# Optimization experiments

Measured on AMD Instinct MI355X. Metric: run time of the kernel, lower is better.

Reference implementation:

```python
import jax, jax.numpy as jnp
import numpy as np

B, S, NX, NH = 4, 1024, 1024, 16
HD = NX // NH  # head_features = 64


def setup_inputs() -> dict:
    key = jax.random.key(0)
    k1, k2, k3 = jax.random.split(key, 3)
    x = jax.random.normal(k1, (B, S, NX), dtype=jnp.float32)
    w_attn = 0.02 * jax.random.normal(k2, (NX, 3 * NX), dtype=jnp.float32)
    b_attn = jnp.zeros((3 * NX,), dtype=jnp.float32)
    w_proj = 0.02 * jax.random.normal(k3, (NX, NX), dtype=jnp.float32)
    b_proj = jnp.zeros((NX,), dtype=jnp.float32)
    causal_bias = jnp.tril(jnp.ones((S, S), dtype=jnp.float32))  # tril buffer
    return {"x": x, "w_attn": w_attn, "b_attn": b_attn,
            "w_proj": w_proj, "b_proj": b_proj, "causal_bias": causal_bias}


def reference(x, w_attn, b_attn, w_proj, b_proj, causal_bias):
    # c_attn: fused qkv projection (Conv1D == addmm)
    qkv = x @ w_attn + b_attn                     # [B, S, 3*NX]
    q, k, v = jnp.split(qkv, 3, axis=-1)          # each [B, S, NX]
    # split heads -> [B, H, S, D]
    q = q.reshape(B, S, NH, HD).transpose(0, 2, 1, 3)
    k = k.reshape(B, S, NH, HD).transpose(0, 2, 1, 3)
    v = v.reshape(B, S, NH, HD).transpose(0, 2, 1, 3)
    # present: stack of (key in [B,H,S,D] layout, value)
    present = jnp.stack((k, v))                   # [2, B, H, S, D]
    # scores with scale=True
    w = jnp.einsum('bhqd,bhkd->bhqk', q, k) / jnp.sqrt(jnp.float32(HD))
    b = causal_bias[None, None, :, :]             # [1,1,S,S] (nd==ns==S)
    w = w * b - 1e10 * (1.0 - b)                  # multiplicative mask trick
    p = jax.nn.softmax(w, axis=-1)
    a = jnp.einsum('bhqk,bhkd->bhqd', p, v)       # [B, H, S, D]
    a = a.transpose(0, 2, 1, 3).reshape(B, S, NX)  # merge heads
    out = a @ w_proj + b_proj                     # c_proj
    return out, present
```

## Files before the change

kernel.cpp:

```cpp
#include <hip/hip_runtime.h>
#include <hip/hip_bf16.h>

typedef __attribute__((ext_vector_type(8))) short short8;
typedef __attribute__((ext_vector_type(4))) float floatx4;

constexpr int Bsz = 4, Ssz = 1024, NXc = 1024, NHc = 16, HDc = 64;
constexpr int OUT_ELEMS  = Bsz * Ssz * NXc;
constexpr int HEAD_ELEMS = Bsz * NHc * Ssz * HDc;

union BF8 { __hip_bfloat16 h[8]; uint4 v; short8 s; };

__device__ __forceinline__ uint4 cvt8(const float* __restrict__ p) {
    float4 a = *reinterpret_cast<const float4*>(p);
    float4 b = *reinterpret_cast<const float4*>(p + 4);
    BF8 u;
    u.h[0] = __float2bfloat16(a.x); u.h[1] = __float2bfloat16(a.y);
    u.h[2] = __float2bfloat16(a.z); u.h[3] = __float2bfloat16(a.w);
    u.h[4] = __float2bfloat16(b.x); u.h[5] = __float2bfloat16(b.y);
    u.h[6] = __float2bfloat16(b.z); u.h[7] = __float2bfloat16(b.w);
    return u.v;
}

__device__ __forceinline__ void load_lds_16B(const void* g, void* l) {
    __builtin_amdgcn_global_load_lds(
        (const __attribute__((address_space(1))) unsigned int*)g,
        (__attribute__((address_space(3))) unsigned int*)l, 16, 0, 0);
}


__global__ __launch_bounds__(256) void prep_kernel(
    const float* __restrict__ x, __hip_bfloat16* __restrict__ x_bf,
    const float* __restrict__ w_attn, __hip_bfloat16* __restrict__ wTa,
    const float* __restrict__ w_proj, __hip_bfloat16* __restrict__ wTp)
{
    const int bid = blockIdx.x, tid = threadIdx.x;
    __shared__ float t[64][65];
    if (bid < 2048) {
        const int i = (bid * 256 + tid) * 8;
        *reinterpret_cast<uint4*>(x_bf + i) = cvt8(x + i);
        return;
    }
    const float* in; __hip_bfloat16* outp; int N, bx, by;
    if (bid < 2816) { const int q = bid - 2048; in = w_attn; outp = wTa; N = 3072; bx = q % 48; by = q / 48; }
    else            { const int q = bid - 2816; in = w_proj; outp = wTp; N = 1024; bx = q % 16; by = q / 16; }
    const int k0 = by * 64, n0 = bx * 64;
#pragma unroll
    for (int j = 0; j < 16; ++j) {
        const int idx = tid + j * 256;
        const int row = idx >> 6, col = idx & 63;
        t[row][col] = in[(size_t)(k0 + row) * N + n0 + col];
    }
    __syncthreads();
#pragma unroll
    for (int j = 0; j < 16; ++j) {
        const int idx = tid + j * 256;
        const int orow = idx >> 6, ocol = idx & 63;
        outp[(size_t)(n0 + orow) * 1024 + k0 + ocol] = __float2bfloat16(t[ocol][orow]);
    }
}

template <int EPI>
__global__ __launch_bounds__(256) void gemm128p(
    const __hip_bfloat16* __restrict__ A,
    const __hip_bfloat16* __restrict__ Bt,
    const float* __restrict__ bias,
    float* __restrict__ outf,
    __hip_bfloat16* __restrict__ qws,
    float* __restrict__ present,
    __hip_bfloat16* __restrict__ kws,
    __hip_bfloat16* __restrict__ vtws,
    int M, int N, int K)
{
    __shared__ __align__(16) __hip_bfloat16 As[3][4096];
    __shared__ __align__(16) __hip_bfloat16 Bs[3][4096];

    const int tid  = threadIdx.x;
    const int w    = tid >> 6, lane = tid & 63;
    const int quad = lane >> 4, l16 = lane & 15;
    const int m0 = blockIdx.y * 128, n0 = blockIdx.x * 128;
    const int mb = (w >> 1) * 64, nbw = (w & 1) * 64;

    const int srow = lane >> 2;
    const int sksw = (((lane & 3) ^ ((lane >> 3) & 3))) * 8;

    const int rsw = (l16 >> 1) & 3;

    floatx4 acc[4][4];
#pragma unroll
    for (int i = 0; i < 4; ++i)
#pragma unroll
        for (int j = 0; j < 4; ++j)
#pragma unroll
            for (int r = 0; r < 4; ++r) acc[i][j][r] = 0.f;

    auto stage = [&](int buf, int k0) {
#pragma unroll
        for (int c = 0; c < 2; ++c) {
            const int chunk = w * 2 + c;
            const int row = chunk * 16 + srow;
            load_lds_16B(A + (size_t)(m0 + row) * K + k0 + sksw,
                         &As[buf][chunk * 512]);
            load_lds_16B(Bt + (size_t)(n0 + row) * K + k0 + sksw,
                         &Bs[buf][chunk * 512]);
        }
    };

    stage(0, 0);
    int cb = 0;
    for (int k0 = 0; k0 < K; k0 += 32) {
        if (k0 + 32 < K) {
            const int nb_ = (cb == 2) ? 0 : cb + 1;
            stage(nb_, k0 + 32);
            asm volatile("s_waitcnt vmcnt(4)" ::: "memory");
        } else {
            asm volatile("s_waitcnt vmcnt(0)" ::: "memory");
        }
        __builtin_amdgcn_s_barrier();
        __builtin_amdgcn_sched_barrier(0);

        short8 af[4], bfr[4];
#pragma unroll
        for (int mi = 0; mi < 4; ++mi)
            af[mi] = *reinterpret_cast<const short8*>(
                &As[cb][(mb + mi * 16 + l16) * 32 + ((quad ^ rsw) * 8)]);
#pragma unroll
        for (int ni = 0; ni < 4; ++ni)
            bfr[ni] = *reinterpret_cast<const short8*>(
                &Bs[cb][(nbw + ni * 16 + l16) * 32 + ((quad ^ rsw) * 8)]);
        __builtin_amdgcn_s_setprio(1);
#pragma unroll
        for (int mi = 0; mi < 4; ++mi)
#pragma unroll
            for (int ni = 0; ni < 4; ++ni)
                acc[mi][ni] = __builtin_amdgcn_mfma_f32_16x16x32_bf16(
                    af[mi], bfr[ni], acc[mi][ni], 0, 0, 0);
        __builtin_amdgcn_s_setprio(0);

        cb = (cb == 2) ? 0 : cb + 1;
    }

#pragma unroll
    for (int mi = 0; mi < 4; ++mi) {
#pragma unroll
        for (int ni = 0; ni < 4; ++ni) {
            const int col = n0 + nbw + ni * 16 + l16;
            const float bsv = bias[col];
#pragma unroll
            for (int r = 0; r < 4; ++r) {
                const int row = m0 + mb + mi * 16 + quad * 4 + r;
                const float v = acc[mi][ni][r] + bsv;
                if (EPI == 0) {
                    const int seg = col >> 10;
                    const int c = col & 1023;
                    if (seg == 0) {
                        qws[(size_t)row * 1024 + c] = __float2bfloat16(v);
                    } else {
                        const int bq = row >> 10, s = row & 1023;
                        const int hh = c >> 6, d = c & 63;
                        const size_t idx =
                            ((size_t)((bq * 16 + hh) * 1024 + s)) * 64 + d;
                        const int kt = s >> 6, key = s & 63;
                        const size_t tbase =
                            ((size_t)((bq * 16 + hh) * 16 + kt)) * 4096;
                        if (seg == 1) {
                            present[idx] = v;
                            kws[tbase + key * 64 +
                                ((((d >> 3) ^ (key & 7)) << 3) | (d & 7))] =
                                __float2bfloat16(v);
                        } else {
                            present[HEAD_ELEMS + idx] = v;
                            vtws[tbase + d * 64 +
                                ((((key >> 3) ^ (d & 7)) << 3) | (key & 7))] =
                                __float2bfloat16(v);
                        }
                    }
                } else {
                    outf[(size_t)row * N + col] = v;
                }
            }
        }
    }
}

__global__ __launch_bounds__(256) void attn_v4(
    const __hip_bfloat16* __restrict__ q_ws,
    const __hip_bfloat16* __restrict__ k_ws,
    const __hip_bfloat16* __restrict__ vt_ws,
    __hip_bfloat16* __restrict__ a_ws)
{
    const int bx = blockIdx.x, h = blockIdx.y, b = blockIdx.z;
    const int tid  = threadIdx.x;
    const int wave = tid >> 6, lane = tid & 63;
    const int quad = lane >> 4, l16 = lane & 15;
    const int stripe = wave * 16;

    const int bh = b * 16 + h;
    const __hip_bfloat16* Kbase = k_ws  + (size_t)bh * 65536;
    const __hip_bfloat16* Vbase = vt_ws + (size_t)bh * 65536;

    __shared__ __align__(16) __hip_bfloat16 Ksf[3][4096];
    __shared__ __align__(16) __hip_bfloat16 Vsf[3][4096];
    __shared__ __align__(16) __hip_bfloat16 Ps[64][72];

    constexpr float SCL = 0.18033688011f;

#pragma unroll
    for (int pass = 0; pass < 2; ++pass) {
        const int qt = (pass == 0) ? (8 + bx) : (7 - bx);

        const __hip_bfloat16* Qb =
            q_ws + ((size_t)(b * Ssz + qt * 64 + stripe + l16)) * NXc + h * 64;
        const short8 qf0 = *reinterpret_cast<const short8*>(Qb + quad * 8);
        const short8 qf1 = *reinterpret_cast<const short8*>(Qb + 32 + quad * 8);

        float m_i[4], l_i[4];
#pragma unroll
        for (int r = 0; r < 4; ++r) { m_i[r] = -1e9f; l_i[r] = 0.f; }
        floatx4 oacc[4];
#pragma unroll
        for (int ni = 0; ni < 4; ++ni)
#pragma unroll
            for (int r = 0; r < 4; ++r) oacc[ni][r] = 0.f;

#pragma unroll
        for (int c2 = 0; c2 < 2; ++c2) {
            const int c = wave + c2 * 4;
            load_lds_16B(Kbase + c * 512 + (lane << 3), &Ksf[0][c * 512]);
            load_lds_16B(Vbase + c * 512 + (lane << 3), &Vsf[0][c * 512]);
        }

        int cw = 0;
        for (int kt = 0; kt <= qt; ++kt) {
            if (kt < qt) {
                const int nb_ = (cw == 2) ? 0 : cw + 1;
                const __hip_bfloat16* Kt = Kbase + (size_t)(kt + 1) * 4096;
                const __hip_bfloat16* Vt = Vbase + (size_t)(kt + 1) * 4096;
#pragma unroll
                for (int c2 = 0; c2 < 2; ++c2) {
                    const int c = wave + c2 * 4;
                    load_lds_16B(Kt + c * 512 + (lane << 3), &Ksf[nb_][c * 512]);
                    load_lds_16B(Vt + c * 512 + (lane << 3), &Vsf[nb_][c * 512]);
                }
                asm volatile("s_waitcnt vmcnt(4)" ::: "memory");
            } else {
                asm volatile("s_waitcnt vmcnt(0)" ::: "memory");
            }
            __builtin_amdgcn_s_barrier();
            __builtin_amdgcn_sched_barrier(0);

            floatx4 sacc[4];
#pragma unroll
            for (int ni = 0; ni < 4; ++ni)
#pragma unroll
                for (int r = 0; r < 4; ++r) sacc[ni][r] = 0.f;
            __builtin_amdgcn_s_setprio(1);
#pragma unroll
            for (int ni = 0; ni < 4; ++ni) {
                const int key = ni * 16 + l16;
                const int sw = key & 7;
                const short8 kf0 = *reinterpret_cast<const short8*>(
                    &Ksf[cw][key * 64 + ((quad ^ sw) << 3)]);
                const short8 kf1 = *reinterpret_cast<const short8*>(
                    &Ksf[cw][key * 64 + (((4 + quad) ^ sw) << 3)]);
                sacc[ni] = __builtin_amdgcn_mfma_f32_16x16x32_bf16(
                    qf0, kf0, sacc[ni], 0, 0, 0);
                sacc[ni] = __builtin_amdgcn_mfma_f32_16x16x32_bf16(
                    qf1, kf1, sacc[ni], 0, 0, 0);
            }
            __builtin_amdgcn_s_setprio(0);

            const bool diag = (kt == qt);
            float alpha_[4];
#pragma unroll
            for (int r = 0; r < 4; ++r) {
                const int lrow = stripe + quad * 4 + r;
                float sv[4];
                float mx = -1e30f;
#pragma unroll
                for (int ni = 0; ni < 4; ++ni) {
                    float v = sacc[ni][r] * SCL;
                    if (diag && (ni * 16 + l16) > lrow) v = -1e9f;
                    sv[ni] = v;
                    mx = fmaxf(mx, v);
                }
                mx = fmaxf(mx, __shfl_xor(mx, 1));
                mx = fmaxf(mx, __shfl_xor(mx, 2));
                mx = fmaxf(mx, __shfl_xor(mx, 4));
                mx = fmaxf(mx, __shfl_xor(mx, 8));
                const float mnew = fmaxf(m_i[r], mx);
                const float al = exp2f(m_i[r] - mnew);
                m_i[r] = mnew;
                float s = 0.f;
#pragma unroll
                for (int nn = 0; nn < 4; ++nn) {
                    const int ni = (nn + quad) & 3;
                    const float p = exp2f(sv[ni] - mnew);
                    s += p;
                    Ps[lrow][ni * 16 + l16] = __float2bfloat16(p);
                }
                s += __shfl_xor(s, 1);
                s += __shfl_xor(s, 2);
                s += __shfl_xor(s, 4);
                s += __shfl_xor(s, 8);
                l_i[r] = l_i[r] * al + s;
                alpha_[r] = al;
            }

#pragma unroll
            for (int ni = 0; ni < 4; ++ni)
#pragma unroll
                for (int r = 0; r < 4; ++r) oacc[ni][r] *= alpha_[r];

            __builtin_amdgcn_s_setprio(1);
#pragma unroll
            for (int kk = 0; kk < 64; kk += 32) {
                const short8 pf = *reinterpret_cast<const short8*>(
                    &Ps[stripe + l16][kk + quad * 8]);
#pragma unroll
                for (int ni = 0; ni < 4; ++ni) {
                    const int d = ni * 16 + l16;
                    const int chunk = (kk >> 3) + quad;
                    const short8 vf = *reinterpret_cast<const short8*>(
                        &Vsf[cw][d * 64 + ((chunk ^ (d & 7)) << 3)]);
                    oacc[ni] = __builtin_amdgcn_mfma_f32_16x16x32_bf16(
                        pf, vf, oacc[ni], 0, 0, 0);
                }
            }
            __builtin_amdgcn_s_setprio(0);

            cw = (cw == 2) ? 0 : cw + 1;
        }

        __builtin_amdgcn_s_barrier();

#pragma unroll
        for (int ni = 0; ni < 4; ++ni) {
#pragma unroll
            for (int r = 0; r < 4; ++r) {
                const int row = qt * 64 + stripe + quad * 4 + r;
                const int col = h * 64 + ni * 16 + l16;
                const float inv = 1.0f / fmaxf(l_i[r], 1e-20f);
                a_ws[((size_t)(b * Ssz + row)) * NXc + col] =
                    __float2bfloat16(oacc[ni][r] * inv);
            }
        }
    }
}

template <int EPI>
__global__ __launch_bounds__(256) void gemm64(
    const void* __restrict__ Av, const float* __restrict__ Bw,
    const float* __restrict__ bias, float* __restrict__ out0,
    float* __restrict__ present, int M, int N, int K)
{
    __shared__ __align__(16) __hip_bfloat16 As[64][40];
    __shared__ __align__(16) __hip_bfloat16 Bs[64][40];
    const int tid = threadIdx.x;
    const int wave = tid >> 6, lane = tid & 63;
    const int quad = lane >> 4, l16 = lane & 15;
    const int m0 = blockIdx.y * 64, n0 = blockIdx.x * 64;
    const int mb = (wave >> 1) * 32, nb = (wave & 1) * 32;
    const int arow = tid >> 2, aseg = tid & 3;
    const int brow = tid >> 3, bseg = tid & 7;
    floatx4 acc[2][2];
#pragma unroll
    for (int i = 0; i < 2; ++i)
#pragma unroll
        for (int j = 0; j < 2; ++j)
#pragma unroll
            for (int r = 0; r < 4; ++r) acc[i][j][r] = 0.f;
    for (int k0 = 0; k0 < K; k0 += 32) {
        if (EPI == 0) {
            const float* A = (const float*)Av;
            *reinterpret_cast<uint4*>(&As[arow][aseg * 8]) =
                cvt8(A + (size_t)(m0 + arow) * K + k0 + aseg * 8);
        } else {
            const __hip_bfloat16* A = (const __hip_bfloat16*)Av;
            *reinterpret_cast<uint4*>(&As[arow][aseg * 8]) =
                *reinterpret_cast<const uint4*>(
                    A + (size_t)(m0 + arow) * K + k0 + aseg * 8);
        }
        const float* bp = Bw + (size_t)(k0 + brow) * N + n0 + bseg * 8;
        float4 b0 = *reinterpret_cast<const float4*>(bp);
        float4 b1 = *reinterpret_cast<const float4*>(bp + 4);
        Bs[bseg * 8 + 0][brow] = __float2bfloat16(b0.x);
        Bs[bseg * 8 + 1][brow] = __float2bfloat16(b0.y);
        Bs[bseg * 8 + 2][brow] = __float2bfloat16(b0.z);
        Bs[bseg * 8 + 3][brow] = __float2bfloat16(b0.w);
        Bs[bseg * 8 + 4][brow] = __float2bfloat16(b1.x);
        Bs[bseg * 8 + 5][brow] = __float2bfloat16(b1.y);
        Bs[bseg * 8 + 6][brow] = __float2bfloat16(b1.z);
        Bs[bseg * 8 + 7][brow] = __float2bfloat16(b1.w);
        __syncthreads();
        short8 af[2], bf[2];
#pragma unroll
        for (int mm = 0; mm < 2; ++mm)
            af[mm] = *reinterpret_cast<const short8*>(&As[mb + mm * 16 + l16][quad * 8]);
#pragma unroll
        for (int nn = 0; nn < 2; ++nn)
            bf[nn] = *reinterpret_cast<const short8*>(&Bs[nb + nn * 16 + l16][quad * 8]);
#pragma unroll
        for (int mm = 0; mm < 2; ++mm)
#pragma unroll
            for (int nn = 0; nn < 2; ++nn)
                acc[mm][nn] = __builtin_amdgcn_mfma_f32_16x16x32_bf16(
                    af[mm], bf[nn], acc[mm][nn], 0, 0, 0);
        __syncthreads();
    }
#pragma unroll
    for (int mm = 0; mm < 2; ++mm)
#pragma unroll
        for (int nn = 0; nn < 2; ++nn) {
            const int col = n0 + nb + nn * 16 + l16;
            const float bsv = bias[col];
#pragma unroll
            for (int r = 0; r < 4; ++r) {
                const int row = m0 + mb + mm * 16 + quad * 4 + r;
                const float v = acc[mm][nn][r] + bsv;
                if (EPI == 0) {
                    const int seg = col >> 10;
                    const int c = col & 1023;
                    if (seg == 0) out0[(size_t)row * 1024 + c] = v;
                    else {
                        const int b = row >> 10, s = row & 1023;
                        const int h = c >> 6, d = c & 63;
                        const size_t idx = ((size_t)((b * 16 + h) * 1024 + s)) * 64 + d;
                        if (seg == 1) present[idx] = v;
                        else          present[HEAD_ELEMS + idx] = v;
                    }
                } else out0[(size_t)row * N + col] = v;
            }
        }
}

__global__ __launch_bounds__(256) void attn64(
    const float* __restrict__ qbuf, const float* __restrict__ present,
    __hip_bfloat16* __restrict__ a_ws)
{
    const int qt = blockIdx.x, h = blockIdx.y, b = blockIdx.z;
    const int tid = threadIdx.x;
    const int wave = tid >> 6, lane = tid & 63;
    const int quad = lane >> 4, l16 = lane & 15;
    const int mb = (wave >> 1) * 32, nb = (wave & 1) * 32;
    const size_t headoff = ((size_t)(b * 16 + h)) * Ssz * HDc;
    const float* Qb = qbuf + ((size_t)(b * Ssz + qt * 64)) * NXc + h * 64;
    const float* Kp = present + headoff;
    const float* Vp = present + HEAD_ELEMS + headoff;
    __shared__ __align__(16) __hip_bfloat16 Qs[64][72];
    __shared__ __align__(16) __hip_bfloat16 Ks[64][72];
    __shared__ __align__(16) __hip_bfloat16 Vts[64][72];
    __shared__ __align__(16) __hip_bfloat16 Ps[64][72];
    __shared__ float Sc[64][65];
    __shared__ float mrow[64], lrow[64], arw[64];
#pragma unroll
    for (int it = 0; it < 2; ++it) {
        const int c = tid + it * 256;
        const int row = c >> 3, seg = c & 7;
        *reinterpret_cast<uint4*>(&Qs[row][seg * 8]) =
            cvt8(Qb + (size_t)row * NXc + seg * 8);
    }
    if (tid < 64) { mrow[tid] = -1e9f; lrow[tid] = 0.f; }
    floatx4 oacc[2][2];
#pragma unroll
    for (int i = 0; i < 2; ++i)
#pragma unroll
        for (int j = 0; j < 2; ++j)
#pragma unroll
            for (int r = 0; r < 4; ++r) oacc[i][j][r] = 0.f;
    __syncthreads();
    for (int kt = 0; kt <= qt; ++kt) {
#pragma unroll
        for (int it = 0; it < 2; ++it) {
            const int c = tid + it * 256;
            const int row = c >> 3, seg = c & 7;
            *reinterpret_cast<uint4*>(&Ks[row][seg * 8]) =
                cvt8(Kp + (size_t)(kt * 64 + row) * 64 + seg * 8);
            const float* vp = Vp + (size_t)(kt * 64 + row) * 64 + seg * 8;
            float4 v0 = *reinterpret_cast<const float4*>(vp);
            float4 v1 = *reinterpret_cast<const float4*>(vp + 4);
            Vts[seg * 8 + 0][row] = __float2bfloat16(v0.x);
            Vts[seg * 8 + 1][row] = __float2bfloat16(v0.y);
            Vts[seg * 8 + 2][row] = __float2bfloat16(v0.z);
            Vts[seg * 8 + 3][row] = __float2bfloat16(v0.w);
            Vts[seg * 8 + 4][row] = __float2bfloat16(v1.x);
            Vts[seg * 8 + 5][row] = __float2bfloat16(v1.y);
            Vts[seg * 8 + 6][row] = __float2bfloat16(v1.z);
            Vts[seg * 8 + 7][row] = __float2bfloat16(v1.w);
        }
        __syncthreads();
        floatx4 sacc[2][2];
#pragma unroll
        for (int i = 0; i < 2; ++i)
#pragma unroll
            for (int j = 0; j < 2; ++j)
#pragma unroll
                for (int r = 0; r < 4; ++r) sacc[i][j][r] = 0.f;
#pragma unroll
        for (int kd = 0; kd < 64; kd += 32) {
            short8 af[2], bf[2];
#pragma unroll
            for (int mm = 0; mm < 2; ++mm)
                af[mm] = *reinterpret_cast<const short8*>(&Qs[mb + mm * 16 + l16][kd + quad * 8]);
#pragma unroll
            for (int nn = 0; nn < 2; ++nn)
                bf[nn] = *reinterpret_cast<const short8*>(&Ks[nb + nn * 16 + l16][kd + quad * 8]);
#pragma unroll
            for (int mm = 0; mm < 2; ++mm)
#pragma unroll
                for (int nn = 0; nn < 2; ++nn)
                    sacc[mm][nn] = __builtin_amdgcn_mfma_f32_16x16x32_bf16(
                        af[mm], bf[nn], sacc[mm][nn], 0, 0, 0);
        }
        const bool diag = (kt == qt);
#pragma unroll
        for (int mm = 0; mm < 2; ++mm)
#pragma unroll
            for (int nn = 0; nn < 2; ++nn)
#pragma unroll
                for (int r = 0; r < 4; ++r) {
                    const int row = mb + mm * 16 + quad * 4 + r;
                    const int col = nb + nn * 16 + l16;
                    float v = fminf(fmaxf(sacc[mm][nn][r] * 0.125f, -1e8f), 1e8f);
                    if (diag && col > row) v = -1e9f;
                    Sc[row][col] = v;
                }
        __syncthreads();
        if (tid < 64) {
            const int r = tid;
            const float mo = mrow[r];
            float mx = mo;
            for (int c = 0; c < 64; ++c) mx = fmaxf(mx, Sc[r][c]);
            const float al = (mo <= -5e8f) ? 0.f : __expf(mo - mx);
            float sum = 0.f;
            for (int c = 0; c < 64; ++c) {
                const float sv = Sc[r][c];
                const float p = (sv <= -5e8f) ? 0.f : __expf(sv - mx);
                sum += p;
                Ps[r][c] = __float2bfloat16(p);
            }
            mrow[r] = mx;
            lrow[r] = lrow[r] * al + sum;
            arw[r]  = al;
        }
        __syncthreads();
#pragma unroll
        for (int mm = 0; mm < 2; ++mm) {
            const int rbase = mb + mm * 16 + quad * 4;
#pragma unroll
            for (int r = 0; r < 4; ++r) {
                const float al = arw[rbase + r];
                oacc[mm][0][r] *= al;
                oacc[mm][1][r] *= al;
            }
        }
#pragma unroll
        for (int kk = 0; kk < 64; kk += 32) {
            short8 pf[2], vf[2];
#pragma unroll
            for (int mm = 0; mm < 2; ++mm)
                pf[mm] = *reinterpret_cast<const short8*>(&Ps[mb + mm * 16 + l16][kk + quad * 8]);
#pragma unroll
            for (int nn = 0; nn < 2; ++nn)
                vf[nn] = *reinterpret_cast<const short8*>(&Vts[nb + nn * 16 + l16][kk + quad * 8]);
#pragma unroll
            for (int mm = 0; mm < 2; ++mm)
#pragma unroll
                for (int nn = 0; nn < 2; ++nn)
                    oacc[mm][nn] = __builtin_amdgcn_mfma_f32_16x16x32_bf16(
                        pf[mm], vf[nn], oacc[mm][nn], 0, 0, 0);
        }
        __syncthreads();
    }
#pragma unroll
    for (int mm = 0; mm < 2; ++mm)
#pragma unroll
        for (int nn = 0; nn < 2; ++nn)
#pragma unroll
            for (int r = 0; r < 4; ++r) {
                const int row = mb + mm * 16 + quad * 4 + r;
                const int col = nb + nn * 16 + l16;
                const float inv = 1.0f / fmaxf(lrow[row], 1e-20f);
                a_ws[((size_t)(b * Ssz + qt * 64 + row)) * NXc + h * 64 + col] =
                    __float2bfloat16(oacc[mm][nn][r] * inv);
            }
}

extern "C" void kernel_launch(void* const* d_in, const int* in_sizes, int n_in,
                              void* d_out, int out_size, void* d_ws, size_t ws_size,
                              hipStream_t stream) {
    const float* x      = (const float*)d_in[0];
    const float* w_attn = (const float*)d_in[1];
    const float* b_attn = (const float*)d_in[2];
    const float* w_proj = (const float*)d_in[3];
    const float* b_proj = (const float*)d_in[4];

    float* out     = (float*)d_out;
    float* present = out + OUT_ELEMS;

    const size_t NEED = 32u * 1024u * 1024u;
    if (ws_size >= NEED) {
        __hip_bfloat16* reg1 = (__hip_bfloat16*)d_ws;
        __hip_bfloat16* reg2 = reg1 + 4194304;
        __hip_bfloat16* reg3 = reg2 + 4194304;
        __hip_bfloat16* wTa  = reg3 + 4194304;
        __hip_bfloat16* wTp  = wTa + 3145728;
        __hip_bfloat16* kws  = (__hip_bfloat16*)out;
        __hip_bfloat16* vtws = kws + 4194304;

        prep_kernel<<<3072, 256, 0, stream>>>(x, reg1, w_attn, wTa, w_proj, wTp);

        gemm128p<0><<<dim3(24, 32), 256, 0, stream>>>(
            reg1, wTa, b_attn, nullptr, reg2, present, kws, vtws,
            4096, 3072, 1024);

        attn_v4<<<dim3(8, 16, 4), 256, 0, stream>>>(reg2, kws, vtws, reg2);

        gemm128p<1><<<dim3(8, 32), 256, 0, stream>>>(
            reg2, wTp, b_proj, out, nullptr, nullptr, nullptr, nullptr,
            4096, 1024, 1024);
    } else {
        __hip_bfloat16* a_ws = (__hip_bfloat16*)d_ws;
        hipMemsetAsync(d_ws, 0, (size_t)OUT_ELEMS * sizeof(__hip_bfloat16), stream);
        gemm64<0><<<dim3(48, 64), 256, 0, stream>>>(x, w_attn, b_attn, out, present,
                                                    4096, 3072, 1024);
        attn64<<<dim3(16, 16, 4), 256, 0, stream>>>(out, present, a_ws);
        gemm64<1><<<dim3(16, 64), 256, 0, stream>>>(a_ws, w_proj, b_proj, out, nullptr,
                                                    4096, 1024, 1024);
    }
}
```

Before: 199.9 us.

## Swizzle GEMM/attention block order and split attention into one q-tile per block

The GEMMs now launch a 1D grid and remap block IDs with an XCD-aware swizzle (wg&7 striding), so neighbouring tiles share an XCD and its L2. The attention kernel drops the two-pass paired q-tile scheme. It launches one block per (b,h,q-tile), heaviest tiles first, with the same XCD swizzle, and cuts the LDS ring from three buffers to two with a full vmcnt(0) wait each iteration. This buys finer-grained load balancing and lower LDS use, which may allow more resident blocks. The cost is less overlap of the K/V prefetch with compute.

After: 213.7 us. 1.07x slower.

```diff
diff --git a/kernel.cpp b/kernel.cpp
--- a/kernel.cpp
+++ b/kernel.cpp
@@ -74,15 +74,20 @@
     __shared__ __align__(16) __hip_bfloat16 As[3][4096];
     __shared__ __align__(16) __hip_bfloat16 Bs[3][4096];
 
+    const int nbx = N >> 7;
+    const int nwg = (M >> 7) * nbx;
+    const int wg  = blockIdx.x;
+    const int swz = (wg & 7) * (nwg >> 3) + (wg >> 3);
+    const int by  = swz / nbx, bx = swz % nbx;
+
     const int tid  = threadIdx.x;
     const int w    = tid >> 6, lane = tid & 63;
     const int quad = lane >> 4, l16 = lane & 15;
-    const int m0 = blockIdx.y * 128, n0 = blockIdx.x * 128;
+    const int m0 = by * 128, n0 = bx * 128;
     const int mb = (w >> 1) * 64, nbw = (w & 1) * 64;
 
     const int srow = lane >> 2;
     const int sksw = (((lane & 3) ^ ((lane >> 3) & 3))) * 8;
-
     const int rsw = (l16 >> 1) & 3;
 
     floatx4 acc[4][4];
@@ -182,167 +187,163 @@
     }
 }
 
-__global__ __launch_bounds__(256) void attn_v4(
+__global__ __launch_bounds__(256) void attn_v5(
     const __hip_bfloat16* __restrict__ q_ws,
     const __hip_bfloat16* __restrict__ k_ws,
     const __hip_bfloat16* __restrict__ vt_ws,
     __hip_bfloat16* __restrict__ a_ws)
 {
-    const int bx = blockIdx.x, h = blockIdx.y, b = blockIdx.z;
+    const int wg  = blockIdx.x;
+    const int swz = (wg & 7) * 128 + (wg >> 3);
+    const int qt  = 15 - (swz & 15);
+    const int bh  = swz >> 4;
+    const int b = bh >> 4, h = bh & 15;
+
     const int tid  = threadIdx.x;
     const int wave = tid >> 6, lane = tid & 63;
     const int quad = lane >> 4, l16 = lane & 15;
     const int stripe = wave * 16;
 
-    const int bh = b * 16 + h;
     const __hip_bfloat16* Kbase = k_ws  + (size_t)bh * 65536;
     const __hip_bfloat16* Vbase = vt_ws + (size_t)bh * 65536;
 
-    __shared__ __align__(16) __hip_bfloat16 Ksf[3][4096];
-    __shared__ __align__(16) __hip_bfloat16 Vsf[3][4096];
+    __shared__ __align__(16) __hip_bfloat16 Ksf[2][4096];
+    __shared__ __align__(16) __hip_bfloat16 Vsf[2][4096];
     __shared__ __align__(16) __hip_bfloat16 Ps[64][72];
 
     constexpr float SCL = 0.18033688011f;
 
-#pragma unroll
-    for (int pass = 0; pass < 2; ++pass) {
-        const int qt = (pass == 0) ? (8 + bx) : (7 - bx);
-
-        const __hip_bfloat16* Qb =
-            q_ws + ((size_t)(b * Ssz + qt * 64 + stripe + l16)) * NXc + h * 64;
-        const short8 qf0 = *reinterpret_cast<const short8*>(Qb + quad * 8);
-        const short8 qf1 = *reinterpret_cast<const short8*>(Qb + 32 + quad * 8);
-
-        float m_i[4], l_i[4];
-#pragma unroll
-        for (int r = 0; r < 4; ++r) { m_i[r] = -1e9f; l_i[r] = 0.f; }
-        floatx4 oacc[4];
+    const __hip_bfloat16* Qb =
+        q_ws + ((size_t)(b * Ssz + qt * 64 + stripe + l16)) * NXc + h * 64;
+    const short8 qf0 = *reinterpret_cast<const short8*>(Qb + quad * 8);
+    const short8 qf1 = *reinterpret_cast<const short8*>(Qb + 32 + quad * 8);
+
+    float m_i[4], l_i[4];
+#pragma unroll
+    for (int r = 0; r < 4; ++r) { m_i[r] = -1e9f; l_i[r] = 0.f; }
+    floatx4 oacc[4];
+#pragma unroll
+    for (int ni = 0; ni < 4; ++ni)
+#pragma unroll
+        for (int r = 0; r < 4; ++r) oacc[ni][r] = 0.f;
+
+#pragma unroll
+    for (int c2 = 0; c2 < 2; ++c2) {
+        const int c = wave + c2 * 4;
+        load_lds_16B(Kbase + c * 512 + (lane << 3), &Ksf[0][c * 512]);
+        load_lds_16B(Vbase + c * 512 + (lane << 3), &Vsf[0][c * 512]);
+    }
+
+    int cw = 0;
+    for (int kt = 0; kt <= qt; ++kt) {
+        asm volatile("s_waitcnt vmcnt(0)" ::: "memory");
+        __builtin_amdgcn_s_barrier();
+        __builtin_amdgcn_sched_barrier(0);
+
+        if (kt < qt) {
+            const __hip_bfloat16* Kt = Kbase + (size_t)(kt + 1) * 4096;
+            const __hip_bfloat16* Vt = Vbase + (size_t)(kt + 1) * 4096;
+            const int nb_ = cw ^ 1;
+#pragma unroll
+            for (int c2 = 0; c2 < 2; ++c2) {
+                const int c = wave + c2 * 4;
+                load_lds_16B(Kt + c * 512 + (lane << 3), &Ksf[nb_][c * 512]);
+                load_lds_16B(Vt + c * 512 + (lane << 3), &Vsf[nb_][c * 512]);
+            }
+        }
+
+        floatx4 sacc[4];
 #pragma unroll
         for (int ni = 0; ni < 4; ++ni)
 #pragma unroll
-            for (int r = 0; r < 4; ++r) oacc[ni][r] = 0.f;
-
-#pragma unroll
-        for (int c2 = 0; c2 < 2; ++c2) {
-            const int c = wave + c2 * 4;
-            load_lds_16B(Kbase + c * 512 + (lane << 3), &Ksf[0][c * 512]);
-            load_lds_16B(Vbase + c * 512 + (lane << 3), &Vsf[0][c * 512]);
-        }
-
-        int cw = 0;
-        for (int kt = 0; kt <= qt; ++kt) {
-            if (kt < qt) {
-                const int nb_ = (cw == 2) ? 0 : cw + 1;
-                const __hip_bfloat16* Kt = Kbase + (size_t)(kt + 1) * 4096;
-                const __hip_bfloat16* Vt = Vbase + (size_t)(kt + 1) * 4096;
-#pragma unroll
-                for (int c2 = 0; c2 < 2; ++c2) {
-                    const int c = wave + c2 * 4;
-                    load_lds_16B(Kt + c * 512 + (lane << 3), &Ksf[nb_][c * 512]);
-                    load_lds_16B(Vt + c * 512 + (lane << 3), &Vsf[nb_][c * 512]);
-                }
-                asm volatile("s_waitcnt vmcnt(4)" ::: "memory");
-            } else {
-                asm volatile("s_waitcnt vmcnt(0)" ::: "memory");
-            }
-            __builtin_amdgcn_s_barrier();
-            __builtin_amdgcn_sched_barrier(0);
-
-            floatx4 sacc[4];
-#pragma unroll
-            for (int ni = 0; ni < 4; ++ni)
-#pragma unroll
-                for (int r = 0; r < 4; ++r) sacc[ni][r] = 0.f;
-            __builtin_amdgcn_s_setprio(1);
+            for (int r = 0; r < 4; ++r) sacc[ni][r] = 0.f;
+        __builtin_amdgcn_s_setprio(1);
+#pragma unroll
+        for (int ni = 0; ni < 4; ++ni) {
+            const int key = ni * 16 + l16;
+            const int sw = key & 7;
+            const short8 kf0 = *reinterpret_cast<const short8*>(
+                &Ksf[cw][key * 64 + ((quad ^ sw) << 3)]);
+            const short8 kf1 = *reinterpret_cast<const short8*>(
+                &Ksf[cw][key * 64 + (((4 + quad) ^ sw) << 3)]);
+            sacc[ni] = __builtin_amdgcn_mfma_f32_16x16x32_bf16(
+                qf0, kf0, sacc[ni], 0, 0, 0);
+            sacc[ni] = __builtin_amdgcn_mfma_f32_16x16x32_bf16(
+                qf1, kf1, sacc[ni], 0, 0, 0);
+        }
+        __builtin_amdgcn_s_setprio(0);
+
+        const bool diag = (kt == qt);
+        float alpha_[4];
+#pragma unroll
+        for (int r = 0; r < 4; ++r) {
+            const int lrow = stripe + quad * 4 + r;
+            float sv[4];
+            float mx = -1e30f;
 #pragma unroll
             for (int ni = 0; ni < 4; ++ni) {
-                const int key = ni * 16 + l16;
-                const int sw = key & 7;
-                const short8 kf0 = *reinterpret_cast<const short8*>(
-                    &Ksf[cw][key * 64 + ((quad ^ sw) << 3)]);
-                const short8 kf1 = *reinterpret_cast<const short8*>(
-                    &Ksf[cw][key * 64 + (((4 + quad) ^ sw) << 3)]);
-                sacc[ni] = __builtin_amdgcn_mfma_f32_16x16x32_bf16(
-                    qf0, kf0, sacc[ni], 0, 0, 0);
-                sacc[ni] = __builtin_amdgcn_mfma_f32_16x16x32_bf16(
-                    qf1, kf1, sacc[ni], 0, 0, 0);
-            }
-            __builtin_amdgcn_s_setprio(0);
-
-            const bool diag = (kt == qt);
-            float alpha_[4];
-#pragma unroll
-            for (int r = 0; r < 4; ++r) {
-                const int lrow = stripe + quad * 4 + r;
-                float sv[4];
-                float mx = -1e30f;
-#pragma unroll
-                for (int ni = 0; ni < 4; ++ni) {
-                    float v = sacc[ni][r] * SCL;
-                    if (diag && (ni * 16 + l16) > lrow) v = -1e9f;
-                    sv[ni] = v;
-                    mx = fmaxf(mx, v);
-                }
-                mx = fmaxf(mx, __shfl_xor(mx, 1));
-                mx = fmaxf(mx, __shfl_xor(mx, 2));
-                mx = fmaxf(mx, __shfl_xor(mx, 4));
-                mx = fmaxf(mx, __shfl_xor(mx, 8));
-                const float mnew = fmaxf(m_i[r], mx);
-                const float al = exp2f(m_i[r] - mnew);
-                m_i[r] = mnew;
-                float s = 0.f;
-#pragma unroll
-                for (int nn = 0; nn < 4; ++nn) {
-                    const int ni = (nn + quad) & 3;
-                    const float p = exp2f(sv[ni] - mnew);
-                    s += p;
-                    Ps[lrow][ni * 16 + l16] = __float2bfloat16(p);
-                }
-                s += __shfl_xor(s, 1);
-                s += __shfl_xor(s, 2);
-                s += __shfl_xor(s, 4);
-                s += __shfl_xor(s, 8);
-                l_i[r] = l_i[r] * al + s;
-                alpha_[r] = al;
-            }
-
-#pragma unroll
-            for (int ni = 0; ni < 4; ++ni)
-#pragma unroll
-                for (int r = 0; r < 4; ++r) oacc[ni][r] *= alpha_[r];
-
-            __builtin_amdgcn_s_setprio(1);
-#pragma unroll
-            for (int kk = 0; kk < 64; kk += 32) {
-                const short8 pf = *reinterpret_cast<const short8*>(
-                    &Ps[stripe + l16][kk + quad * 8]);
-#pragma unroll
-                for (int ni = 0; ni < 4; ++ni) {
-                    const int d = ni * 16 + l16;
-                    const int chunk = (kk >> 3) + quad;
-                    const short8 vf = *reinterpret_cast<const short8*>(
-                        &Vsf[cw][d * 64 + ((chunk ^ (d & 7)) << 3)]);
-                    oacc[ni] = __builtin_amdgcn_mfma_f32_16x16x32_bf16(
-                        pf, vf, oacc[ni], 0, 0, 0);
-                }
-            }
-            __builtin_amdgcn_s_setprio(0);
-
-            cw = (cw == 2) ? 0 : cw + 1;
-        }
-
-        __builtin_amdgcn_s_barrier();
-
-#pragma unroll
-        for (int ni = 0; ni < 4; ++ni) {
-#pragma unroll
-            for (int r = 0; r < 4; ++r) {
-                const int row = qt * 64 + stripe + quad * 4 + r;
-                const int col = h * 64 + ni * 16 + l16;
-                const float inv = 1.0f / fmaxf(l_i[r], 1e-20f);
-                a_ws[((size_t)(b * Ssz + row)) * NXc + col] =
-                    __float2bfloat16(oacc[ni][r] * inv);
-            }
+                float v = sacc[ni][r] * SCL;
+                if (diag && (ni * 16 + l16) > lrow) v = -1e9f;
+                sv[ni] = v;
+                mx = fmaxf(mx, v);
+            }
+            mx = fmaxf(mx, __shfl_xor(mx, 1));
+            mx = fmaxf(mx, __shfl_xor(mx, 2));
+            mx = fmaxf(mx, __shfl_xor(mx, 4));
+            mx = fmaxf(mx, __shfl_xor(mx, 8));
+            const float mnew = fmaxf(m_i[r], mx);
+            const float al = exp2f(m_i[r] - mnew);
+            m_i[r] = mnew;
+            float s = 0.f;
+#pragma unroll
+            for (int nn = 0; nn < 4; ++nn) {
+                const int ni = (nn + quad) & 3;
+                const float p = exp2f(sv[ni] - mnew);
+                s += p;
+                Ps[lrow][ni * 16 + l16] = __float2bfloat16(p);
+            }
+            s += __shfl_xor(s, 1);
+            s += __shfl_xor(s, 2);
+            s += __shfl_xor(s, 4);
+            s += __shfl_xor(s, 8);
+            l_i[r] = l_i[r] * al + s;
+            alpha_[r] = al;
+        }
+
+#pragma unroll
+        for (int ni = 0; ni < 4; ++ni)
+#pragma unroll
+            for (int r = 0; r < 4; ++r) oacc[ni][r] *= alpha_[r];
+
+        __builtin_amdgcn_s_setprio(1);
+#pragma unroll
+        for (int kk = 0; kk < 64; kk += 32) {
+            const short8 pf = *reinterpret_cast<const short8*>(
+                &Ps[stripe + l16][kk + quad * 8]);
+#pragma unroll
+            for (int ni = 0; ni < 4; ++ni) {
+                const int d = ni * 16 + l16;
+                const int chunk = (kk >> 3) + quad;
+                const short8 vf = *reinterpret_cast<const short8*>(
+                    &Vsf[cw][d * 64 + ((chunk ^ (d & 7)) << 3)]);
+                oacc[ni] = __builtin_amdgcn_mfma_f32_16x16x32_bf16(
+                    pf, vf, oacc[ni], 0, 0, 0);
+            }
+        }
+        __builtin_amdgcn_s_setprio(0);
+
+        cw ^= 1;
+    }
+
+#pragma unroll
+    for (int ni = 0; ni < 4; ++ni) {
+#pragma unroll
+        for (int r = 0; r < 4; ++r) {
+            const int row = qt * 64 + stripe + quad * 4 + r;
+            const int col = h * 64 + ni * 16 + l16;
+            const float inv = 1.0f / fmaxf(l_i[r], 1e-20f);
+            a_ws[((size_t)(b * Ssz + row)) * NXc + col] =
+                __float2bfloat16(oacc[ni][r] * inv);
         }
     }
 }
@@ -609,13 +610,13 @@
 
         prep_kernel<<<3072, 256, 0, stream>>>(x, reg1, w_attn, wTa, w_proj, wTp);
 
-        gemm128p<0><<<dim3(24, 32), 256, 0, stream>>>(
+        gemm128p<0><<<768, 256, 0, stream>>>(
             reg1, wTa, b_attn, nullptr, reg2, present, kws, vtws,
             4096, 3072, 1024);
 
-        attn_v4<<<dim3(8, 16, 4), 256, 0, stream>>>(reg2, kws, vtws, reg2);
-
-        gemm128p<1><<<dim3(8, 32), 256, 0, stream>>>(
+        attn_v5<<<1024, 256, 0, stream>>>(reg2, kws, vtws, reg2);
+
+        gemm128p<1><<<256, 256, 0, stream>>>(
             reg2, wTp, b_proj, out, nullptr, nullptr, nullptr, nullptr,
             4096, 1024, 1024);
     } else {
```
